# Optimization experiments

Hardware: AMD Instinct MI355X
Metric: run time of the kernel (lower is better)

Reference implementation:

```python
import jax, jax.numpy as jnp
import numpy as np

B, T, C, H = 256, 512, 64, 512


def _init(key, shape, scale=0.05):
    return jax.random.normal(key, shape, dtype=jnp.float32) * scale


def setup_inputs() -> dict:
    key = jax.random.key(0)
    ks = jax.random.split(key, 12)
    return {
        "x": jax.random.normal(ks[0], (B, T, C), dtype=jnp.float32),
        # encoder GRU params (PyTorch layout: W_ih [3H, C], W_hh [3H, H])
        "enc_Wih": _init(ks[1], (3 * H, C)),
        "enc_Whh": _init(ks[2], (3 * H, H)),
        "enc_bih": _init(ks[3], (3 * H,)),
        "enc_bhh": _init(ks[4], (3 * H,)),
        # decoder GRU params
        "dec_Wih": _init(ks[5], (3 * H, C)),
        "dec_Whh": _init(ks[6], (3 * H, H)),
        "dec_bih": _init(ks[7], (3 * H,)),
        "dec_bhh": _init(ks[8], (3 * H,)),
        # output projection
        "Wout": _init(ks[9], (C, H)),
        "bout": _init(ks[10], (C,)),
    }


def _gru_cell(gi, h, Whh, bhh):
    # PyTorch GRU math: r,z,n gate order
    gh = h @ Whh.T + bhh
    ir, iz, inn = jnp.split(gi, 3, axis=-1)
    hr, hz, hn = jnp.split(gh, 3, axis=-1)
    r = jax.nn.sigmoid(ir + hr)
    z = jax.nn.sigmoid(iz + hz)
    n = jnp.tanh(inn + r * hn)
    return (1.0 - z) * n + z * h


def reference(x, enc_Wih, enc_Whh, enc_bih, enc_bhh,
              dec_Wih, dec_Whh, dec_bih, dec_bhh, Wout, bout):
    b, t, c = x.shape
    hdim = enc_Whh.shape[1]
    # ---- encoder: single full-sequence GRU, return final hidden ----
    xs = jnp.swapaxes(x, 0, 1)                      # [T, B, C]
    gi_all = xs @ enc_Wih.T + enc_bih               # precompute input gates [T, B, 3H]

    def enc_step(h, gi):
        return _gru_cell(gi, h, enc_Whh, enc_bhh), None

    h0 = jnp.zeros((b, hdim), dtype=x.dtype)
    h_enc, _ = jax.lax.scan(enc_step, h0, gi_all)

    # ---- decoder: free-running (eval mode, teacher_forcing_ratio=0) ----
    start = jnp.zeros((b, c), dtype=x.dtype)        # zero start token

    def dec_step(carry, _):
        prev, h = carry
        gi = prev @ dec_Wih.T + dec_bih
        h_new = _gru_cell(gi, h, dec_Whh, dec_bhh)
        pred = h_new @ Wout.T + bout                # [B, C]
        return (pred, h_new), pred

    _, preds = jax.lax.scan(dec_step, (start, h_enc), None, length=t)
    return jnp.swapaxes(preds, 0, 1)                # [B, T, C]
```

## Files before the change

kernel.cpp:

```cpp
#include <hip/hip_runtime.h>
#include <hip/hip_bf16.h>


#define B_ 256
#define T_ 512
#define C_ 64
#define H_ 512
#define TC_ 32768
#define BH_ 131072

typedef __attribute__((ext_vector_type(8))) short s16x8;
typedef __attribute__((ext_vector_type(4))) float f32x4;
typedef __attribute__((ext_vector_type(4))) unsigned int u32x4;

__device__ __forceinline__ unsigned short f2b(float f) {
    unsigned int u = __float_as_uint(f);
    unsigned int r = (u + 0x7FFFu + ((u >> 16) & 1u)) >> 16;
    return (unsigned short)r;
}
__device__ __forceinline__ float sigm(float v) {
    return __builtin_amdgcn_rcpf(1.f + __expf(-v));
}
__device__ __forceinline__ float ftanh(float v) {
    float a = fabsf(v);
    float e = __expf(-2.f * a);
    float t = (1.f - e) * __builtin_amdgcn_rcpf(1.f + e);
    return copysignf(t, v);
}
__device__ __forceinline__ s16x8 ldh16a(const unsigned short* p) {
    u32x4 r;
    asm volatile("global_load_dwordx4 %0, %1, off sc0 sc1"
                 : "=v"(r) : "v"(p));
    return __builtin_bit_cast(s16x8, r);
}
__device__ __forceinline__ void sth16a(unsigned short* p, u32x4 v) {
    asm volatile("global_store_dwordx4 %0, %1, off sc0 sc1"
                 :: "v"(p), "v"(v) : "memory");
}


__global__ __launch_bounds__(256) void prep_enc_k(
    const float* __restrict__ Wih, const float* __restrict__ Whh,
    const float* __restrict__ bih, const float* __restrict__ bhh,
    unsigned short* __restrict__ W, float* __restrict__ bias)
{
    int idx = blockIdx.x * 256 + threadIdx.x;
    if (idx >= 2048 * 576) return;
    int n = idx / 576, k = idx % 576;
    int part = (n >> 4) & 3, jc = n & 15, j16 = n >> 6;
    int j = j16 * 16 + jc;
    float v;
    if (part == 0)      v = (k < 64) ? Wih[j * 64 + k]          : Whh[(size_t)j * 512 + (k - 64)];
    else if (part == 1) v = (k < 64) ? Wih[(512 + j) * 64 + k]  : Whh[(size_t)(512 + j) * 512 + (k - 64)];
    else if (part == 2) v = (k < 64) ? Wih[(1024 + j) * 64 + k] : 0.f;
    else                v = (k < 64) ? 0.f                       : Whh[(size_t)(1024 + j) * 512 + (k - 64)];
    W[(size_t)n * 576 + k] = f2b(v);
    if (k == 0) {
        float b;
        if (part == 0)      b = bih[j] + bhh[j];
        else if (part == 1) b = bih[512 + j] + bhh[512 + j];
        else if (part == 2) b = bih[1024 + j];
        else                b = bhh[1024 + j];
        bias[n] = b;
    }
}

__global__ __launch_bounds__(256) void prep_dec_k(
    const float* __restrict__ Wih, const float* __restrict__ Whh,
    const float* __restrict__ Wout,
    unsigned short* __restrict__ W1, unsigned short* __restrict__ W0)
{
    int n = blockIdx.x;
    __shared__ float wrow[64];
    bool isout = (n >= 2048);
    int part = 0, j = 0, n3 = 0;
    if (!isout) {
        part = (n >> 4) & 3;
        int jc = n & 15, j16 = n >> 6;
        j = j16 * 16 + jc;
        n3 = (part == 0) ? j : (part == 1) ? (512 + j) : (1024 + j);
    }
    if (threadIdx.x < 64 && !isout && part != 3)
        wrow[threadIdx.x] = Wih[n3 * 64 + threadIdx.x];
    __syncthreads();
    for (int kk = 0; kk < 2; ++kk) {
        int k = kk * 256 + threadIdx.x;
        float v1, v0;
        if (isout) {
            v1 = v0 = Wout[(size_t)(n - 2048) * 512 + k];
        } else if (part == 3) {
            v1 = v0 = Whh[(size_t)(1024 + j) * 512 + k];
        } else {
            float af = 0.f;
            #pragma unroll
            for (int c = 0; c < 64; ++c) af += wrow[c] * Wout[(size_t)c * 512 + k];
            if (part == 2) { v1 = af; v0 = 0.f; }
            else { float wh = Whh[(size_t)n3 * 512 + k]; v1 = af + wh; v0 = wh; }
        }
        W1[(size_t)n * 512 + k] = f2b(v1);
        W0[(size_t)n * 512 + k] = f2b(v0);
    }
}

__global__ __launch_bounds__(256) void prep_dec_bias_k(
    const float* __restrict__ Wih, const float* __restrict__ bih,
    const float* __restrict__ bhh, const float* __restrict__ bout,
    float* __restrict__ b1, float* __restrict__ b0)
{
    int n = blockIdx.x * 256 + threadIdx.x;
    if (n >= 2112) return;
    if (n >= 2048) { b1[n] = bout[n - 2048]; b0[n] = bout[n - 2048]; return; }
    int part = (n >> 4) & 3, jc = n & 15, j16 = n >> 6;
    int j = j16 * 16 + jc;
    float v1, v0;
    if (part == 3) { v1 = v0 = bhh[1024 + j]; }
    else {
        int n3 = (part == 0) ? j : (part == 1) ? (512 + j) : (1024 + j);
        float wib = 0.f;
        #pragma unroll
        for (int c = 0; c < 64; ++c) wib += Wih[n3 * 64 + c] * bout[c];
        if (part == 2) { v1 = bih[1024 + j] + wib; v0 = bih[1024 + j]; }
        else { float base = bih[n3] + bhh[n3]; v1 = base + wib; v0 = base; }
    }
    b1[n] = v1; b0[n] = v0;
}


template<bool SLEEP>
__device__ __forceinline__ void wait_flags32(const unsigned int* fl, int lane, unsigned int tgt) {
    const unsigned int* fp = fl + (lane & 31) * 32;
    while (true) {
        unsigned int fv = __hip_atomic_load(fp, __ATOMIC_RELAXED, __HIP_MEMORY_SCOPE_AGENT);
        if (__all(fv >= tgt)) break;
        if (SLEEP) __builtin_amdgcn_s_sleep(1);
    }
    asm volatile("" ::: "memory");
    __builtin_amdgcn_sched_barrier(0);
}

template<int NK, bool PRED>
__device__ __forceinline__ void do_step(
    const unsigned short* __restrict__ hin, unsigned short* __restrict__ hout,
    const s16x8 (&bfr)[36], const s16x8 (&pfr)[8], const float4 (&xf)[2][2],
    const float* bR, float bp, float (&h32)[4],
    float* __restrict__ out, int tout,
    unsigned int* __restrict__ flagp, int step,
    int r0, int j, int kh, int rh, int lane, bool duty,
    float (*Ored)[64][28], unsigned short (*Hst)[16][24])
{
    constexpr int HK = NK / 2;
    const int jc = lane & 15, kq = lane >> 4;
    const int ks0 = kh * HK;
    const unsigned short* hrow = hin + (size_t)(r0 + rh * 16 + jc) * H_;

    s16x8 af[HK];
    if (NK == 18 && kh == 0) {
        #pragma unroll
        for (int i2 = 0; i2 < 2; ++i2) {
            s16x8 v;
            v[0] = (short)f2b(xf[i2][0].x); v[1] = (short)f2b(xf[i2][0].y);
            v[2] = (short)f2b(xf[i2][0].z); v[3] = (short)f2b(xf[i2][0].w);
            v[4] = (short)f2b(xf[i2][1].x); v[5] = (short)f2b(xf[i2][1].y);
            v[6] = (short)f2b(xf[i2][1].z); v[7] = (short)f2b(xf[i2][1].w);
            af[i2] = v;
        }
    }
    #pragma unroll
    for (int i = 0; i < HK; ++i) {
        const int gks = ks0 + i;
        const bool isx = (NK == 18) && (gks < 2);
        if (!isx) {
            const int hk = ((NK == 18) ? (gks - 2) : gks) * 32 + kq * 8;
            af[i] = ldh16a(hrow + hk);
        }
    }
    asm volatile("s_waitcnt vmcnt(0)" ::: "memory");
    __builtin_amdgcn_sched_barrier(0);

    f32x4 acc[4] = {{0,0,0,0},{0,0,0,0},{0,0,0,0},{0,0,0,0}};
    f32x4 pacc = {0,0,0,0};
    #pragma unroll
    for (int i = 0; i < HK; ++i) {
        #pragma unroll
        for (int q = 0; q < 4; ++q)
            acc[q] = __builtin_amdgcn_mfma_f32_16x16x32_bf16(af[i], bfr[i * 4 + q], acc[q], 0, 0, 0);
        if (PRED && duty)
            pacc = __builtin_amdgcn_mfma_f32_16x16x32_bf16(af[i], pfr[i], pacc, 0, 0, 0);
    }

    if (kh == 1) {
        #pragma unroll
        for (int q = 0; q < 4; ++q) *(f32x4*)&Ored[rh][lane][q * 4] = acc[q];
        if (PRED && duty) *(f32x4*)&Ored[rh][lane][16] = pacc;
    }
    asm volatile("s_waitcnt lgkmcnt(0)" ::: "memory");
    __builtin_amdgcn_s_barrier();
    __builtin_amdgcn_sched_barrier(0);

    if (kh == 0) {
        #pragma unroll
        for (int q = 0; q < 4; ++q) {
            f32x4 o = *(const f32x4*)&Ored[rh][lane][q * 4];
            acc[q] = acc[q] + o;
        }
        if (PRED && duty) {
            f32x4 o = *(const f32x4*)&Ored[rh][lane][16];
            pacc = pacc + o;
        }
        float hn[4];
        #pragma unroll
        for (int r = 0; r < 4; ++r) {
            float gr = acc[0][r] + bR[0];
            float gz = acc[1][r] + bR[1];
            float gi = acc[2][r] + bR[2];
            float gh = acc[3][r] + bR[3];
            float rg = sigm(gr), zg = sigm(gz);
            float ng = ftanh(gi + rg * gh);
            hn[r] = (1.f - zg) * ng + zg * h32[r];
            h32[r] = hn[r];
        }
        #pragma unroll
        for (int r = 0; r < 4; ++r) Hst[rh][kq * 4 + r][jc] = f2b(hn[r]);
    }
    asm volatile("s_waitcnt lgkmcnt(0)" ::: "memory");
    __builtin_amdgcn_s_barrier();
    __builtin_amdgcn_sched_barrier(0);

    if (kh == 0 && rh == 0) {
        const int row = lane >> 1, half = lane & 1;
        u32x4 hv = *(const u32x4*)&Hst[row >> 4][row & 15][half * 8];
        sth16a(hout + (size_t)(r0 + row) * H_ + j * 16 + half * 8, hv);
        asm volatile("s_waitcnt vmcnt(0)" ::: "memory");
        if (lane == 0)
            __hip_atomic_store(flagp, (unsigned int)(step + 1),
                               __ATOMIC_RELAXED, __HIP_MEMORY_SCOPE_AGENT);
    }
    if (PRED && kh == 0 && duty) {
        #pragma unroll
        for (int r = 0; r < 4; ++r)
            out[(size_t)(r0 + rh * 16 + kq * 4 + r) * TC_ + (size_t)tout * C_ + j * 16 + jc] = pacc[r] + bp;
    }
}

__global__ __launch_bounds__(256, 1) void gru_persist(
    const unsigned short* __restrict__ WencT,
    const unsigned short* __restrict__ WdecT,
    const unsigned short* __restrict__ Wdec0T,
    const float* __restrict__ benc, const float* __restrict__ bdec, const float* __restrict__ bdec0,
    const float* __restrict__ x,
    unsigned short* __restrict__ h16,
    float* __restrict__ out,
    unsigned int* __restrict__ flags)
{
    __shared__ __align__(16) float Ored[2][64][28];
    __shared__ __align__(16) unsigned short Hst[2][16][24];

    const int bid = blockIdx.x;
    const int g = bid & 7, j = bid >> 3;
    const int tid = threadIdx.x;
    const int w = tid >> 6, lane = tid & 63;
    const int kh = w & 1, rh = w >> 1;
    const int jc = lane & 15, kq = lane >> 4;
    const int r0 = g * 32;
    const bool duty = (j < 4);
    unsigned int* fl = flags + g * 32 * 32;
    unsigned int* flagp = fl + j * 32;

    float be[4], bd[4], bd0[4];
    #pragma unroll
    for (int q = 0; q < 4; ++q) {
        be[q]  = benc[j * 64 + q * 16 + jc];
        bd[q]  = bdec[j * 64 + q * 16 + jc];
        bd0[q] = bdec0[j * 64 + q * 16 + jc];
    }
    const float bp = duty ? bdec[2048 + j * 16 + jc] : 0.f;

    s16x8 bfr[36];
    #pragma unroll
    for (int i = 0; i < 9; ++i) {
        const int gks = kh * 9 + i;
        #pragma unroll
        for (int q = 0; q < 4; ++q)
            bfr[i * 4 + q] = *(const s16x8*)(WencT + (size_t)(j * 64 + q * 16 + jc) * 576 + gks * 32 + kq * 8);
    }
    s16x8 pfr[8];
    #pragma unroll
    for (int i = 0; i < 8; ++i) pfr[i] = s16x8{0,0,0,0,0,0,0,0};

    float h32[4] = {0.f, 0.f, 0.f, 0.f};
    int parity = 0;
    float4 xf[2][2];

    for (int step = 0; step < 1024; ++step) {
        const bool enc = step < 512;
        if (enc && kh == 0) {
            const float* xp = x + (size_t)(r0 + rh * 16 + jc) * TC_ + (size_t)step * C_ + kq * 8;
            #pragma unroll
            for (int i2 = 0; i2 < 2; ++i2) {
                xf[i2][0] = *(const float4*)(xp + i2 * 32);
                xf[i2][1] = *(const float4*)(xp + i2 * 32 + 4);
            }
        }
        if (step == 512) {
            #pragma unroll
            for (int i = 0; i < 8; ++i) {
                const int gks = kh * 8 + i;
                #pragma unroll
                for (int q = 0; q < 4; ++q)
                    bfr[i * 4 + q] = *(const s16x8*)(Wdec0T + (size_t)(j * 64 + q * 16 + jc) * 512 + gks * 32 + kq * 8);
                if (duty)
                    pfr[i] = *(const s16x8*)(WdecT + (size_t)(2048 + j * 16 + jc) * 512 + gks * 32 + kq * 8);
            }
        } else if (step == 513) {
            #pragma unroll
            for (int i = 0; i < 8; ++i) {
                const int gks = kh * 8 + i;
                #pragma unroll
                for (int q = 0; q < 4; ++q)
                    bfr[i * 4 + q] = *(const s16x8*)(WdecT + (size_t)(j * 64 + q * 16 + jc) * 512 + gks * 32 + kq * 8);
            }
        }
        if (step > 0) {
            if (w == 1) wait_flags32<false>(fl, lane, (unsigned int)step);
            __builtin_amdgcn_s_barrier();
            __builtin_amdgcn_sched_barrier(0);
        }

        const unsigned short* hin = h16 + (size_t)parity * BH_;
        unsigned short* hout = h16 + (size_t)(parity ^ 1) * BH_;

        if (enc)
            do_step<18, false>(hin, hout, bfr, pfr, xf, be,  bp, h32, out, 0,
                               flagp, step, r0, j, kh, rh, lane, duty, Ored, Hst);
        else if (step == 512)
            do_step<16, false>(hin, hout, bfr, pfr, xf, bd0, bp, h32, out, 0,
                               flagp, step, r0, j, kh, rh, lane, duty, Ored, Hst);
        else
            do_step<16, true >(hin, hout, bfr, pfr, xf, bd,  bp, h32, out, step - 513,
                               flagp, step, r0, j, kh, rh, lane, duty, Ored, Hst);

        parity ^= 1;
    }

    if (duty) {
        wait_flags32<true>(fl, lane, 1024u);
        const unsigned short* hin = h16 + (size_t)parity * BH_;
        const unsigned short* hrow = hin + (size_t)(r0 + rh * 16 + jc) * H_;
        s16x8 hf[8];
        #pragma unroll
        for (int i = 0; i < 8; ++i) {
            const int gks = kh * 8 + i;
            hf[i] = ldh16a(hrow + gks * 32 + kq * 8);
        }
        asm volatile("s_waitcnt vmcnt(0)" ::: "memory");
        __builtin_amdgcn_sched_barrier(0);
        f32x4 pacc = {0, 0, 0, 0};
        #pragma unroll
        for (int i = 0; i < 8; ++i)
            pacc = __builtin_amdgcn_mfma_f32_16x16x32_bf16(hf[i], pfr[i], pacc, 0, 0, 0);
        if (kh == 1) *(f32x4*)&Ored[rh][lane][16] = pacc;
        asm volatile("s_waitcnt lgkmcnt(0)" ::: "memory");
        __builtin_amdgcn_s_barrier();
        __builtin_amdgcn_sched_barrier(0);
        if (kh == 0) {
            f32x4 o = *(const f32x4*)&Ored[rh][lane][16];
            pacc = pacc + o;
            #pragma unroll
            for (int r = 0; r < 4; ++r)
                out[(size_t)(r0 + rh * 16 + kq * 4 + r) * TC_ + (size_t)511 * C_ + j * 16 + jc] = pacc[r] + bp;
        }
    }
}


extern "C" void kernel_launch(void* const* d_in, const int* in_sizes, int n_in,
                              void* d_out, int out_size, void* d_ws, size_t ws_size,
                              hipStream_t stream) {
    const float* x    = (const float*)d_in[0];
    const float* eWih = (const float*)d_in[1];
    const float* eWhh = (const float*)d_in[2];
    const float* ebih = (const float*)d_in[3];
    const float* ebhh = (const float*)d_in[4];
    const float* dWih = (const float*)d_in[5];
    const float* dWhh = (const float*)d_in[6];
    const float* dbih = (const float*)d_in[7];
    const float* dbhh = (const float*)d_in[8];
    const float* Wout = (const float*)d_in[9];
    const float* bout = (const float*)d_in[10];

    size_t off = 0;
    auto carve = [&](size_t bytes) -> void* {
        off = (off + 255) & ~(size_t)255;
        void* p = (char*)d_ws + off;
        off += bytes;
        return p;
    };
    unsigned short* WencT  = (unsigned short*)carve((size_t)2048 * 576 * 2);
    unsigned short* WdecT  = (unsigned short*)carve((size_t)2112 * 512 * 2);
    unsigned short* Wdec0T = (unsigned short*)carve((size_t)2112 * 512 * 2);
    float* benc  = (float*)carve(2048 * 4);
    float* bdec  = (float*)carve(2112 * 4);
    float* bdec0 = (float*)carve(2112 * 4);
    unsigned short* h16 = (unsigned short*)carve((size_t)2 * BH_ * 2);
    unsigned int* flags = (unsigned int*)carve(8 * 32 * 32 * 4);

    hipMemsetAsync(h16, 0, (size_t)2 * BH_ * 2, stream);
    hipMemsetAsync(flags, 0, 8 * 32 * 32 * 4, stream);

    prep_enc_k<<<(2048 * 576 + 255) / 256, 256, 0, stream>>>(eWih, eWhh, ebih, ebhh, WencT, benc);
    prep_dec_k<<<2112, 256, 0, stream>>>(dWih, dWhh, Wout, WdecT, Wdec0T);
    prep_dec_bias_k<<<9, 256, 0, stream>>>(dWih, dbih, dbhh, bout, bdec, bdec0);

    gru_persist<<<256, 256, 0, stream>>>(WencT, WdecT, Wdec0T, benc, bdec, bdec0,
                                         x, h16, (float*)d_out, flags);
}
```

Before: 3.255 ms.

## Detect same-XCD groups to use cheaper cache scope and per-wave flags

```diff
diff --git a/kernel.cpp b/kernel.cpp
--- a/kernel.cpp
+++ b/kernel.cpp
@@ -27,15 +27,21 @@
     float t = (1.f - e) * __builtin_amdgcn_rcpf(1.f + e);
     return copysignf(t, v);
 }
-__device__ __forceinline__ s16x8 ldh16a(const unsigned short* p) {
+template<bool FAST>
+__device__ __forceinline__ s16x8 ldh16x(const unsigned short* p) {
     u32x4 r;
-    asm volatile("global_load_dwordx4 %0, %1, off sc0 sc1"
-                 : "=v"(r) : "v"(p));
+    if constexpr (FAST)
+        asm volatile("global_load_dwordx4 %0, %1, off sc0" : "=v"(r) : "v"(p));
+    else
+        asm volatile("global_load_dwordx4 %0, %1, off sc0 sc1" : "=v"(r) : "v"(p));
     return __builtin_bit_cast(s16x8, r);
 }
-__device__ __forceinline__ void sth16a(unsigned short* p, u32x4 v) {
-    asm volatile("global_store_dwordx4 %0, %1, off sc0 sc1"
-                 :: "v"(p), "v"(v) : "memory");
+template<bool FAST>
+__device__ __forceinline__ void sth16x(unsigned short* p, u32x4 v) {
+    if constexpr (FAST)
+        asm volatile("global_store_dwordx4 %0, %1, off sc0" :: "v"(p), "v"(v) : "memory");
+    else
+        asm volatile("global_store_dwordx4 %0, %1, off sc0 sc1" :: "v"(p), "v"(v) : "memory");
 }
 
 
@@ -127,8 +133,8 @@
 
 
 template<bool SLEEP>
-__device__ __forceinline__ void wait_flags32(const unsigned int* fl, int lane, unsigned int tgt) {
-    const unsigned int* fp = fl + (lane & 31) * 32;
+__device__ __forceinline__ void wait_flags64(const unsigned int* fl, int lane, unsigned int tgt) {
+    const unsigned int* fp = fl + lane * 32;
     while (true) {
         unsigned int fv = __hip_atomic_load(fp, __ATOMIC_RELAXED, __HIP_MEMORY_SCOPE_AGENT);
         if (__all(fv >= tgt)) break;
@@ -138,7 +144,7 @@
     __builtin_amdgcn_sched_barrier(0);
 }
 
-template<int NK, bool PRED>
+template<int NK, bool PRED, bool FAST>
 __device__ __forceinline__ void do_step(
     const unsigned short* __restrict__ hin, unsigned short* __restrict__ hout,
     const s16x8 (&bfr)[36], const s16x8 (&pfr)[8], const float4 (&xf)[2][2],
@@ -171,7 +177,7 @@
         const bool isx = (NK == 18) && (gks < 2);
         if (!isx) {
             const int hk = ((NK == 18) ? (gks - 2) : gks) * 32 + kq * 8;
-            af[i] = ldh16a(hrow + hk);
+            af[i] = ldh16x<FAST>(hrow + hk);
         }
     }
     asm volatile("s_waitcnt vmcnt(0)" ::: "memory");
@@ -221,72 +227,40 @@
         }
         #pragma unroll
         for (int r = 0; r < 4; ++r) Hst[rh][kq * 4 + r][jc] = f2b(hn[r]);
-    }
-    asm volatile("s_waitcnt lgkmcnt(0)" ::: "memory");
-    __builtin_amdgcn_s_barrier();
-    __builtin_amdgcn_sched_barrier(0);
-
-    if (kh == 0 && rh == 0) {
-        const int row = lane >> 1, half = lane & 1;
-        u32x4 hv = *(const u32x4*)&Hst[row >> 4][row & 15][half * 8];
-        sth16a(hout + (size_t)(r0 + row) * H_ + j * 16 + half * 8, hv);
+        asm volatile("s_waitcnt lgkmcnt(0)" ::: "memory");
+        __builtin_amdgcn_sched_barrier(0);
+        if (lane < 32) {
+            const int row = lane >> 1, hh = lane & 1;
+            u32x4 hv = *(const u32x4*)&Hst[rh][row][hh * 8];
+            sth16x<FAST>(hout + (size_t)(r0 + rh * 16 + row) * H_ + j * 16 + hh * 8, hv);
+        }
         asm volatile("s_waitcnt vmcnt(0)" ::: "memory");
         if (lane == 0)
             __hip_atomic_store(flagp, (unsigned int)(step + 1),
                                __ATOMIC_RELAXED, __HIP_MEMORY_SCOPE_AGENT);
-    }
-    if (PRED && kh == 0 && duty) {
-        #pragma unroll
-        for (int r = 0; r < 4; ++r)
-            out[(size_t)(r0 + rh * 16 + kq * 4 + r) * TC_ + (size_t)tout * C_ + j * 16 + jc] = pacc[r] + bp;
-    }
-}
-
-__global__ __launch_bounds__(256, 1) void gru_persist(
-    const unsigned short* __restrict__ WencT,
+        if (PRED && duty) {
+            #pragma unroll
+            for (int r = 0; r < 4; ++r)
+                out[(size_t)(r0 + rh * 16 + kq * 4 + r) * TC_ + (size_t)tout * C_ + j * 16 + jc] = pacc[r] + bp;
+        }
+    }
+}
+
+template<bool FAST>
+__device__ __forceinline__ void persist_body(
     const unsigned short* __restrict__ WdecT,
     const unsigned short* __restrict__ Wdec0T,
-    const float* __restrict__ benc, const float* __restrict__ bdec, const float* __restrict__ bdec0,
     const float* __restrict__ x,
     unsigned short* __restrict__ h16,
     float* __restrict__ out,
-    unsigned int* __restrict__ flags)
-{
-    __shared__ __align__(16) float Ored[2][64][28];
-    __shared__ __align__(16) unsigned short Hst[2][16][24];
-
-    const int bid = blockIdx.x;
-    const int g = bid & 7, j = bid >> 3;
-    const int tid = threadIdx.x;
-    const int w = tid >> 6, lane = tid & 63;
-    const int kh = w & 1, rh = w >> 1;
+    unsigned int* __restrict__ fl,
+    s16x8 (&bfr)[36], s16x8 (&pfr)[8],
+    const float (&be)[4], const float (&bd)[4], const float (&bd0)[4], float bp,
+    int r0, int j, int w, int kh, int rh, int lane, bool duty,
+    float (*Ored)[64][28], unsigned short (*Hst)[16][24])
+{
     const int jc = lane & 15, kq = lane >> 4;
-    const int r0 = g * 32;
-    const bool duty = (j < 4);
-    unsigned int* fl = flags + g * 32 * 32;
-    unsigned int* flagp = fl + j * 32;
-
-    float be[4], bd[4], bd0[4];
-    #pragma unroll
-    for (int q = 0; q < 4; ++q) {
-        be[q]  = benc[j * 64 + q * 16 + jc];
-        bd[q]  = bdec[j * 64 + q * 16 + jc];
-        bd0[q] = bdec0[j * 64 + q * 16 + jc];
-    }
-    const float bp = duty ? bdec[2048 + j * 16 + jc] : 0.f;
-
-    s16x8 bfr[36];
-    #pragma unroll
-    for (int i = 0; i < 9; ++i) {
-        const int gks = kh * 9 + i;
-        #pragma unroll
-        for (int q = 0; q < 4; ++q)
-            bfr[i * 4 + q] = *(const s16x8*)(WencT + (size_t)(j * 64 + q * 16 + jc) * 576 + gks * 32 + kq * 8);
-    }
-    s16x8 pfr[8];
-    #pragma unroll
-    for (int i = 0; i < 8; ++i) pfr[i] = s16x8{0,0,0,0,0,0,0,0};
-
+    unsigned int* flagp = fl + (j * 2 + rh) * 32;
     float h32[4] = {0.f, 0.f, 0.f, 0.f};
     int parity = 0;
     float4 xf[2][2];
@@ -321,7 +295,7 @@
             }
         }
         if (step > 0) {
-            if (w == 1) wait_flags32<false>(fl, lane, (unsigned int)step);
+            if (w == 1) wait_flags64<false>(fl, lane, (unsigned int)step);
             __builtin_amdgcn_s_barrier();
             __builtin_amdgcn_sched_barrier(0);
         }
@@ -330,27 +304,27 @@
         unsigned short* hout = h16 + (size_t)(parity ^ 1) * BH_;
 
         if (enc)
-            do_step<18, false>(hin, hout, bfr, pfr, xf, be,  bp, h32, out, 0,
-                               flagp, step, r0, j, kh, rh, lane, duty, Ored, Hst);
+            do_step<18, false, FAST>(hin, hout, bfr, pfr, xf, be,  bp, h32, out, 0,
+                                     flagp, step, r0, j, kh, rh, lane, duty, Ored, Hst);
         else if (step == 512)
-            do_step<16, false>(hin, hout, bfr, pfr, xf, bd0, bp, h32, out, 0,
-                               flagp, step, r0, j, kh, rh, lane, duty, Ored, Hst);
+            do_step<16, false, FAST>(hin, hout, bfr, pfr, xf, bd0, bp, h32, out, 0,
+                                     flagp, step, r0, j, kh, rh, lane, duty, Ored, Hst);
         else
-            do_step<16, true >(hin, hout, bfr, pfr, xf, bd,  bp, h32, out, step - 513,
-                               flagp, step, r0, j, kh, rh, lane, duty, Ored, Hst);
+            do_step<16, true,  FAST>(hin, hout, bfr, pfr, xf, bd,  bp, h32, out, step - 513,
+                                     flagp, step, r0, j, kh, rh, lane, duty, Ored, Hst);
 
         parity ^= 1;
     }
 
     if (duty) {
-        wait_flags32<true>(fl, lane, 1024u);
+        wait_flags64<true>(fl, lane, 1024u);
         const unsigned short* hin = h16 + (size_t)parity * BH_;
         const unsigned short* hrow = hin + (size_t)(r0 + rh * 16 + jc) * H_;
         s16x8 hf[8];
         #pragma unroll
         for (int i = 0; i < 8; ++i) {
             const int gks = kh * 8 + i;
-            hf[i] = ldh16a(hrow + gks * 32 + kq * 8);
+            hf[i] = ldh16x<FAST>(hrow + gks * 32 + kq * 8);
         }
         asm volatile("s_waitcnt vmcnt(0)" ::: "memory");
         __builtin_amdgcn_sched_barrier(0);
@@ -370,6 +344,75 @@
                 out[(size_t)(r0 + rh * 16 + kq * 4 + r) * TC_ + (size_t)511 * C_ + j * 16 + jc] = pacc[r] + bp;
         }
     }
+}
+
+__global__ __launch_bounds__(256, 1) void gru_persist(
+    const unsigned short* __restrict__ WencT,
+    const unsigned short* __restrict__ WdecT,
+    const unsigned short* __restrict__ Wdec0T,
+    const float* __restrict__ benc, const float* __restrict__ bdec, const float* __restrict__ bdec0,
+    const float* __restrict__ x,
+    unsigned short* __restrict__ h16,
+    float* __restrict__ out,
+    unsigned int* __restrict__ flags,
+    unsigned int* __restrict__ xcdslot)
+{
+    __shared__ __align__(16) float Ored[2][64][28];
+    __shared__ __align__(16) unsigned short Hst[2][16][24];
+
+    const int bid = blockIdx.x;
+    const int g = bid & 7, j = bid >> 3;
+    const int tid = threadIdx.x;
+    const int w = tid >> 6, lane = tid & 63;
+    const int kh = w & 1, rh = w >> 1;
+    const int jc = lane & 15, kq = lane >> 4;
+    const int r0 = g * 32;
+    const bool duty = (j < 4);
+    unsigned int* fl = flags + g * 64 * 32;
+
+    unsigned int xcc;
+    asm volatile("s_getreg_b32 %0, hwreg(HW_REG_XCC_ID)" : "=s"(xcc));
+    if (tid == 0)
+        __hip_atomic_store(xcdslot + bid, xcc + 1u, __ATOMIC_RELAXED, __HIP_MEMORY_SCOPE_AGENT);
+
+    float be[4], bd[4], bd0[4];
+    #pragma unroll
+    for (int q = 0; q < 4; ++q) {
+        be[q]  = benc[j * 64 + q * 16 + jc];
+        bd[q]  = bdec[j * 64 + q * 16 + jc];
+        bd0[q] = bdec0[j * 64 + q * 16 + jc];
+    }
+    const float bp = duty ? bdec[2048 + j * 16 + jc] : 0.f;
+
+    s16x8 bfr[36];
+    #pragma unroll
+    for (int i = 0; i < 9; ++i) {
+        const int gks = kh * 9 + i;
+        #pragma unroll
+        for (int q = 0; q < 4; ++q)
+            bfr[i * 4 + q] = *(const s16x8*)(WencT + (size_t)(j * 64 + q * 16 + jc) * 576 + gks * 32 + kq * 8);
+    }
+    s16x8 pfr[8];
+    #pragma unroll
+    for (int i = 0; i < 8; ++i) pfr[i] = s16x8{0,0,0,0,0,0,0,0};
+
+    unsigned int mv;
+    {
+        const unsigned int* sp = xcdslot + (((lane & 31) << 3) + g);
+        while (true) {
+            mv = __hip_atomic_load(sp, __ATOMIC_RELAXED, __HIP_MEMORY_SCOPE_AGENT);
+            if (!__any(mv == 0u)) break;
+            __builtin_amdgcn_s_sleep(2);
+        }
+    }
+    const bool fast = __all(mv == __builtin_amdgcn_readfirstlane(mv));
+
+    if (fast)
+        persist_body<true>(WdecT, Wdec0T, x, h16, out, fl, bfr, pfr,
+                           be, bd, bd0, bp, r0, j, w, kh, rh, lane, duty, Ored, Hst);
+    else
+        persist_body<false>(WdecT, Wdec0T, x, h16, out, fl, bfr, pfr,
+                            be, bd, bd0, bp, r0, j, w, kh, rh, lane, duty, Ored, Hst);
 }
 
 
@@ -402,15 +445,17 @@
     float* bdec  = (float*)carve(2112 * 4);
     float* bdec0 = (float*)carve(2112 * 4);
     unsigned short* h16 = (unsigned short*)carve((size_t)2 * BH_ * 2);
-    unsigned int* flags = (unsigned int*)carve(8 * 32 * 32 * 4);
+    unsigned int* flags = (unsigned int*)carve(8 * 64 * 32 * 4);
+    unsigned int* xcdslot = (unsigned int*)carve(256 * 4);
 
     hipMemsetAsync(h16, 0, (size_t)2 * BH_ * 2, stream);
-    hipMemsetAsync(flags, 0, 8 * 32 * 32 * 4, stream);
+    hipMemsetAsync(flags, 0, 8 * 64 * 32 * 4, stream);
+    hipMemsetAsync(xcdslot, 0, 256 * 4, stream);
 
     prep_enc_k<<<(2048 * 576 + 255) / 256, 256, 0, stream>>>(eWih, eWhh, ebih, ebhh, WencT, benc);
     prep_dec_k<<<2112, 256, 0, stream>>>(dWih, dWhh, Wout, WdecT, Wdec0T);
     prep_dec_bias_k<<<9, 256, 0, stream>>>(dWih, dbih, dbhh, bout, bdec, bdec0);
 
     gru_persist<<<256, 256, 0, stream>>>(WencT, WdecT, Wdec0T, benc, bdec, bdec0,
-                                         x, h16, (float*)d_out, flags);
-}
+                                         x, h16, (float*)d_out, flags, xcdslot);
+}
```

Result: slower. 3.578 ms (+9.9%).

## Repartition persistent GRU blocks into 16-row groups with 32 hidden units each

Applied to the files above, without the earlier changes.

```diff
diff --git a/kernel.cpp b/kernel.cpp
--- a/kernel.cpp
+++ b/kernel.cpp
@@ -29,13 +29,11 @@
 }
 __device__ __forceinline__ s16x8 ldh16a(const unsigned short* p) {
     u32x4 r;
-    asm volatile("global_load_dwordx4 %0, %1, off sc0 sc1"
-                 : "=v"(r) : "v"(p));
+    asm volatile("global_load_dwordx4 %0, %1, off sc0 sc1" : "=v"(r) : "v"(p));
     return __builtin_bit_cast(s16x8, r);
 }
 __device__ __forceinline__ void sth16a(unsigned short* p, u32x4 v) {
-    asm volatile("global_store_dwordx4 %0, %1, off sc0 sc1"
-                 :: "v"(p), "v"(v) : "memory");
+    asm volatile("global_store_dwordx4 %0, %1, off sc0 sc1" :: "v"(p), "v"(v) : "memory");
 }
 
 
@@ -127,8 +125,8 @@
 
 
 template<bool SLEEP>
-__device__ __forceinline__ void wait_flags32(const unsigned int* fl, int lane, unsigned int tgt) {
-    const unsigned int* fp = fl + (lane & 31) * 32;
+__device__ __forceinline__ void wait_flags16(const unsigned int* fl, int lane, unsigned int tgt) {
+    const unsigned int* fp = fl + (lane & 15) * 32;
     while (true) {
         unsigned int fv = __hip_atomic_load(fp, __ATOMIC_RELAXED, __HIP_MEMORY_SCOPE_AGENT);
         if (__all(fv >= tgt)) break;
@@ -145,13 +143,13 @@
     const float* bR, float bp, float (&h32)[4],
     float* __restrict__ out, int tout,
     unsigned int* __restrict__ flagp, int step,
-    int r0, int j, int kh, int rh, int lane, bool duty,
-    float (*Ored)[64][28], unsigned short (*Hst)[16][24])
+    int r0, int j, int kh, int ch, int lane, bool duty,
+    float (*Ored)[64][20], unsigned short (*Hst)[32])
 {
     constexpr int HK = NK / 2;
     const int jc = lane & 15, kq = lane >> 4;
     const int ks0 = kh * HK;
-    const unsigned short* hrow = hin + (size_t)(r0 + rh * 16 + jc) * H_;
+    const unsigned short* hrow = hin + (size_t)(r0 + jc) * H_;
 
     s16x8 af[HK];
     if (NK == 18 && kh == 0) {
@@ -179,19 +177,20 @@
 
     f32x4 acc[4] = {{0,0,0,0},{0,0,0,0},{0,0,0,0},{0,0,0,0}};
     f32x4 pacc = {0,0,0,0};
+    const bool pduty = PRED && duty && (ch == 0);
     #pragma unroll
     for (int i = 0; i < HK; ++i) {
         #pragma unroll
         for (int q = 0; q < 4; ++q)
             acc[q] = __builtin_amdgcn_mfma_f32_16x16x32_bf16(af[i], bfr[i * 4 + q], acc[q], 0, 0, 0);
-        if (PRED && duty)
+        if (pduty)
             pacc = __builtin_amdgcn_mfma_f32_16x16x32_bf16(af[i], pfr[i], pacc, 0, 0, 0);
     }
 
     if (kh == 1) {
         #pragma unroll
-        for (int q = 0; q < 4; ++q) *(f32x4*)&Ored[rh][lane][q * 4] = acc[q];
-        if (PRED && duty) *(f32x4*)&Ored[rh][lane][16] = pacc;
+        for (int q = 0; q < 4; ++q) *(f32x4*)&Ored[ch][lane][q * 4] = acc[q];
+        if (pduty) *(f32x4*)&Ored[0][lane][16] = pacc;
     }
     asm volatile("s_waitcnt lgkmcnt(0)" ::: "memory");
     __builtin_amdgcn_s_barrier();
@@ -200,11 +199,11 @@
     if (kh == 0) {
         #pragma unroll
         for (int q = 0; q < 4; ++q) {
-            f32x4 o = *(const f32x4*)&Ored[rh][lane][q * 4];
+            f32x4 o = *(const f32x4*)&Ored[ch][lane][q * 4];
             acc[q] = acc[q] + o;
         }
-        if (PRED && duty) {
-            f32x4 o = *(const f32x4*)&Ored[rh][lane][16];
+        if (pduty) {
+            f32x4 o = *(const f32x4*)&Ored[0][lane][16];
             pacc = pacc + o;
         }
         float hn[4];
@@ -220,25 +219,25 @@
             h32[r] = hn[r];
         }
         #pragma unroll
-        for (int r = 0; r < 4; ++r) Hst[rh][kq * 4 + r][jc] = f2b(hn[r]);
+        for (int r = 0; r < 4; ++r) Hst[kq * 4 + r][ch * 16 + jc] = f2b(hn[r]);
     }
     asm volatile("s_waitcnt lgkmcnt(0)" ::: "memory");
     __builtin_amdgcn_s_barrier();
     __builtin_amdgcn_sched_barrier(0);
 
-    if (kh == 0 && rh == 0) {
-        const int row = lane >> 1, half = lane & 1;
-        u32x4 hv = *(const u32x4*)&Hst[row >> 4][row & 15][half * 8];
-        sth16a(hout + (size_t)(r0 + row) * H_ + j * 16 + half * 8, hv);
+    if (kh == 0 && ch == 0) {
+        const int row = lane >> 2, quarter = lane & 3;
+        u32x4 hv = *(const u32x4*)&Hst[row][quarter * 8];
+        sth16a(hout + (size_t)(r0 + row) * H_ + j * 32 + quarter * 8, hv);
         asm volatile("s_waitcnt vmcnt(0)" ::: "memory");
         if (lane == 0)
             __hip_atomic_store(flagp, (unsigned int)(step + 1),
                                __ATOMIC_RELAXED, __HIP_MEMORY_SCOPE_AGENT);
-    }
-    if (PRED && kh == 0 && duty) {
-        #pragma unroll
-        for (int r = 0; r < 4; ++r)
-            out[(size_t)(r0 + rh * 16 + kq * 4 + r) * TC_ + (size_t)tout * C_ + j * 16 + jc] = pacc[r] + bp;
+        if (PRED && duty) {
+            #pragma unroll
+            for (int r = 0; r < 4; ++r)
+                out[(size_t)(r0 + kq * 4 + r) * TC_ + (size_t)tout * C_ + j * 16 + jc] = pacc[r] + bp;
+        }
     }
 }
 
@@ -252,26 +251,27 @@
     float* __restrict__ out,
     unsigned int* __restrict__ flags)
 {
-    __shared__ __align__(16) float Ored[2][64][28];
-    __shared__ __align__(16) unsigned short Hst[2][16][24];
+    __shared__ __align__(16) float Ored[2][64][20];
+    __shared__ __align__(16) unsigned short Hst[16][32];
 
     const int bid = blockIdx.x;
-    const int g = bid & 7, j = bid >> 3;
+    const int g = bid & 15, j = bid >> 4;
     const int tid = threadIdx.x;
-    const int w = tid >> 6, lane = tid & 63;
-    const int kh = w & 1, rh = w >> 1;
+    const int c = tid >> 6, lane = tid & 63;
+    const int kh = c & 1, ch = c >> 1;
     const int jc = lane & 15, kq = lane >> 4;
-    const int r0 = g * 32;
+    const int r0 = g * 16;
     const bool duty = (j < 4);
-    unsigned int* fl = flags + g * 32 * 32;
+    unsigned int* fl = flags + g * 16 * 32;
     unsigned int* flagp = fl + j * 32;
+    const int n0 = j * 128 + ch * 64;
 
     float be[4], bd[4], bd0[4];
     #pragma unroll
     for (int q = 0; q < 4; ++q) {
-        be[q]  = benc[j * 64 + q * 16 + jc];
-        bd[q]  = bdec[j * 64 + q * 16 + jc];
-        bd0[q] = bdec0[j * 64 + q * 16 + jc];
+        be[q]  = benc[n0 + q * 16 + jc];
+        bd[q]  = bdec[n0 + q * 16 + jc];
+        bd0[q] = bdec0[n0 + q * 16 + jc];
     }
     const float bp = duty ? bdec[2048 + j * 16 + jc] : 0.f;
 
@@ -281,7 +281,7 @@
         const int gks = kh * 9 + i;
         #pragma unroll
         for (int q = 0; q < 4; ++q)
-            bfr[i * 4 + q] = *(const s16x8*)(WencT + (size_t)(j * 64 + q * 16 + jc) * 576 + gks * 32 + kq * 8);
+            bfr[i * 4 + q] = *(const s16x8*)(WencT + (size_t)(n0 + q * 16 + jc) * 576 + gks * 32 + kq * 8);
     }
     s16x8 pfr[8];
     #pragma unroll
@@ -294,7 +294,7 @@
     for (int step = 0; step < 1024; ++step) {
         const bool enc = step < 512;
         if (enc && kh == 0) {
-            const float* xp = x + (size_t)(r0 + rh * 16 + jc) * TC_ + (size_t)step * C_ + kq * 8;
+            const float* xp = x + (size_t)(r0 + jc) * TC_ + (size_t)step * C_ + kq * 8;
             #pragma unroll
             for (int i2 = 0; i2 < 2; ++i2) {
                 xf[i2][0] = *(const float4*)(xp + i2 * 32);
@@ -307,8 +307,8 @@
                 const int gks = kh * 8 + i;
                 #pragma unroll
                 for (int q = 0; q < 4; ++q)
-                    bfr[i * 4 + q] = *(const s16x8*)(Wdec0T + (size_t)(j * 64 + q * 16 + jc) * 512 + gks * 32 + kq * 8);
-                if (duty)
+                    bfr[i * 4 + q] = *(const s16x8*)(Wdec0T + (size_t)(n0 + q * 16 + jc) * 512 + gks * 32 + kq * 8);
+                if (duty && ch == 0)
                     pfr[i] = *(const s16x8*)(WdecT + (size_t)(2048 + j * 16 + jc) * 512 + gks * 32 + kq * 8);
             }
         } else if (step == 513) {
@@ -317,11 +317,11 @@
                 const int gks = kh * 8 + i;
                 #pragma unroll
                 for (int q = 0; q < 4; ++q)
-                    bfr[i * 4 + q] = *(const s16x8*)(WdecT + (size_t)(j * 64 + q * 16 + jc) * 512 + gks * 32 + kq * 8);
+                    bfr[i * 4 + q] = *(const s16x8*)(WdecT + (size_t)(n0 + q * 16 + jc) * 512 + gks * 32 + kq * 8);
             }
         }
         if (step > 0) {
-            if (w == 1) wait_flags32<false>(fl, lane, (unsigned int)step);
+            if (c == 1) wait_flags16<false>(fl, lane, (unsigned int)step);
             __builtin_amdgcn_s_barrier();
             __builtin_amdgcn_sched_barrier(0);
         }
@@ -331,43 +331,45 @@
 
         if (enc)
             do_step<18, false>(hin, hout, bfr, pfr, xf, be,  bp, h32, out, 0,
-                               flagp, step, r0, j, kh, rh, lane, duty, Ored, Hst);
+                               flagp, step, r0, j, kh, ch, lane, duty, Ored, Hst);
         else if (step == 512)
             do_step<16, false>(hin, hout, bfr, pfr, xf, bd0, bp, h32, out, 0,
-                               flagp, step, r0, j, kh, rh, lane, duty, Ored, Hst);
+                               flagp, step, r0, j, kh, ch, lane, duty, Ored, Hst);
         else
             do_step<16, true >(hin, hout, bfr, pfr, xf, bd,  bp, h32, out, step - 513,
-                               flagp, step, r0, j, kh, rh, lane, duty, Ored, Hst);
+                               flagp, step, r0, j, kh, ch, lane, duty, Ored, Hst);
 
         parity ^= 1;
     }
 
     if (duty) {
-        wait_flags32<true>(fl, lane, 1024u);
+        wait_flags16<true>(fl, lane, 1024u);
         const unsigned short* hin = h16 + (size_t)parity * BH_;
-        const unsigned short* hrow = hin + (size_t)(r0 + rh * 16 + jc) * H_;
-        s16x8 hf[8];
-        #pragma unroll
-        for (int i = 0; i < 8; ++i) {
-            const int gks = kh * 8 + i;
-            hf[i] = ldh16a(hrow + gks * 32 + kq * 8);
-        }
-        asm volatile("s_waitcnt vmcnt(0)" ::: "memory");
-        __builtin_amdgcn_sched_barrier(0);
+        const unsigned short* hrow = hin + (size_t)(r0 + jc) * H_;
         f32x4 pacc = {0, 0, 0, 0};
-        #pragma unroll
-        for (int i = 0; i < 8; ++i)
-            pacc = __builtin_amdgcn_mfma_f32_16x16x32_bf16(hf[i], pfr[i], pacc, 0, 0, 0);
-        if (kh == 1) *(f32x4*)&Ored[rh][lane][16] = pacc;
+        if (ch == 0) {
+            s16x8 hf[8];
+            #pragma unroll
+            for (int i = 0; i < 8; ++i) {
+                const int gks = kh * 8 + i;
+                hf[i] = ldh16a(hrow + gks * 32 + kq * 8);
+            }
+            asm volatile("s_waitcnt vmcnt(0)" ::: "memory");
+            __builtin_amdgcn_sched_barrier(0);
+            #pragma unroll
+            for (int i = 0; i < 8; ++i)
+                pacc = __builtin_amdgcn_mfma_f32_16x16x32_bf16(hf[i], pfr[i], pacc, 0, 0, 0);
+            if (kh == 1) *(f32x4*)&Ored[0][lane][16] = pacc;
+        }
         asm volatile("s_waitcnt lgkmcnt(0)" ::: "memory");
         __builtin_amdgcn_s_barrier();
         __builtin_amdgcn_sched_barrier(0);
-        if (kh == 0) {
-            f32x4 o = *(const f32x4*)&Ored[rh][lane][16];
+        if (kh == 0 && ch == 0) {
+            f32x4 o = *(const f32x4*)&Ored[0][lane][16];
             pacc = pacc + o;
             #pragma unroll
             for (int r = 0; r < 4; ++r)
-                out[(size_t)(r0 + rh * 16 + kq * 4 + r) * TC_ + (size_t)511 * C_ + j * 16 + jc] = pacc[r] + bp;
+                out[(size_t)(r0 + kq * 4 + r) * TC_ + (size_t)511 * C_ + j * 16 + jc] = pacc[r] + bp;
         }
     }
 }
@@ -402,10 +404,10 @@
     float* bdec  = (float*)carve(2112 * 4);
     float* bdec0 = (float*)carve(2112 * 4);
     unsigned short* h16 = (unsigned short*)carve((size_t)2 * BH_ * 2);
-    unsigned int* flags = (unsigned int*)carve(8 * 32 * 32 * 4);
+    unsigned int* flags = (unsigned int*)carve(16 * 16 * 32 * 4);
 
     hipMemsetAsync(h16, 0, (size_t)2 * BH_ * 2, stream);
-    hipMemsetAsync(flags, 0, 8 * 32 * 32 * 4, stream);
+    hipMemsetAsync(flags, 0, 16 * 16 * 32 * 4, stream);
 
     prep_enc_k<<<(2048 * 576 + 255) / 256, 256, 0, stream>>>(eWih, eWhh, ebih, ebhh, WencT, benc);
     prep_dec_k<<<2112, 256, 0, stream>>>(dWih, dWhh, Wout, WdecT, Wdec0T);
```

After: 3.240 ms. Within noise of the previous version (-0.5%).
